# Performance work log

Hardware: AMD Instinct MI355X
Metric: run time of the kernel (lower is better)

## Reference

```python
import jax, jax.numpy as jnp
import numpy as np

H = 2048       # hidden_size
NH = 16        # num query heads
NKV = 4        # num key/value heads
HD = 128       # head_dim
EPS = 1e-6
ROPE_BASE = 10000.0


def rms_norm(x, w):
    xf = x.astype(jnp.float32)
    var = jnp.mean(xf * xf, axis=-1, keepdims=True)
    return (w * (xf * jax.lax.rsqrt(var + EPS)).astype(x.dtype))


def rope_cos_sin(seq_len, dtype):
    inv_freq = 1.0 / (ROPE_BASE ** (jnp.arange(0, HD, 2, dtype=jnp.float32) / HD))
    pos = jnp.arange(seq_len, dtype=jnp.float32)
    ang = pos[:, None] * inv_freq[None, :]            # [S, HD/2]
    emb = jnp.concatenate([ang, ang], axis=-1)        # [S, HD]
    return jnp.cos(emb).astype(dtype), jnp.sin(emb).astype(dtype)


def rotate_half(x):
    x1, x2 = jnp.split(x, 2, axis=-1)
    return jnp.concatenate([-x2, x1], axis=-1)


def setup_inputs() -> dict:
    key = jax.random.key(0)
    ks = jax.random.split(key, 8)
    B, S = 2, 2048
    hidden_states = jax.random.normal(ks[0], (B, S, H), dtype=jnp.float32)
    # additive causal mask [B,1,S,S]
    causal = jnp.where(jnp.tril(jnp.ones((S, S), dtype=bool)), 0.0, -1e9).astype(jnp.float32)
    attention_mask = jnp.broadcast_to(causal[None, None], (B, 1, S, S))
    sc = 1.0 / np.sqrt(H)
    Wq = jax.random.normal(ks[1], (NH * HD, H), dtype=jnp.float32) * sc
    Wk = jax.random.normal(ks[2], (NKV * HD, H), dtype=jnp.float32) * sc
    Wv = jax.random.normal(ks[3], (NKV * HD, H), dtype=jnp.float32) * sc
    Wo = jax.random.normal(ks[4], (H, NH * HD), dtype=jnp.float32) * sc
    q_norm_w = jnp.ones((HD,), dtype=jnp.float32)
    k_norm_w = jnp.ones((HD,), dtype=jnp.float32)
    return {"hidden_states": hidden_states, "attention_mask": attention_mask,
            "Wq": Wq, "Wk": Wk, "Wv": Wv, "Wo": Wo,
            "q_norm_w": q_norm_w, "k_norm_w": k_norm_w}


def reference(hidden_states, attention_mask, Wq, Wk, Wv, Wo, q_norm_w, k_norm_w):
    B, S, _ = hidden_states.shape
    # projections (nn.Linear: x @ W.T)
    q = (hidden_states @ Wq.T).reshape(B, S, NH, HD).transpose(0, 2, 1, 3)   # [B,NH,S,HD]
    k = (hidden_states @ Wk.T).reshape(B, S, NKV, HD).transpose(0, 2, 1, 3)  # [B,NKV,S,HD]
    v = (hidden_states @ Wv.T).reshape(B, S, NKV, HD).transpose(0, 2, 1, 3)
    # QK RMSNorm over head_dim
    q = rms_norm(q, q_norm_w)
    k = rms_norm(k, k_norm_w)
    # RoPE
    cos, sin = rope_cos_sin(S, q.dtype)        # [S,HD]
    q = q * cos + rotate_half(q) * sin
    k = k * cos + rotate_half(k) * sin
    # GQA: repeat kv heads
    n_rep = NH // NKV
    k = jnp.repeat(k, n_rep, axis=1)           # [B,NH,S,HD]
    v = jnp.repeat(v, n_rep, axis=1)
    # attention
    scores = jnp.einsum('bhqd,bhkd->bhqk', q, k) / np.sqrt(HD)
    scores = scores + attention_mask
    probs = jax.nn.softmax(scores, axis=-1)
    attn = jnp.einsum('bhqk,bhkd->bhqd', probs, v)
    attn = attn.transpose(0, 2, 1, 3).reshape(B, S, NH * HD)
    return attn @ Wo.T
```

## Files before the change

kernel.cpp:

```cpp
#include <hip/hip_runtime.h>
#include <math.h>

#define NH 16
#define NKV 4
#define HD 128
#define SEQ 2048
#define BATCH 2
#define EPSF 1e-6f
#define QKV 3072

typedef __attribute__((ext_vector_type(8))) short bf16x8;
typedef __attribute__((ext_vector_type(4))) short short4v;
typedef __attribute__((ext_vector_type(4))) float f32x4;

__device__ __forceinline__ short f2bf(float x) {
    unsigned u = __float_as_uint(x);
    u += 0x7fffu + ((u >> 16) & 1u);
    return (short)(u >> 16);
}
__device__ __forceinline__ float bf2f(short x) {
    return __uint_as_float((unsigned)(unsigned short)x << 16);
}

__device__ __forceinline__ void gll16(const short* g, short* l) {
    __builtin_amdgcn_global_load_lds(
        (const __attribute__((address_space(1))) unsigned*)g,
        (__attribute__((address_space(3))) unsigned*)l, 16, 0, 0);
}

__global__ __launch_bounds__(256)
void cast_all(const float* __restrict__ hs, const float* __restrict__ Wq,
              const float* __restrict__ Wk, const float* __restrict__ Wv,
              const float* __restrict__ Wo, short* __restrict__ hsb,
              short* __restrict__ wqkv, short* __restrict__ wob)
{
    const size_t MEG = 1024 * 1024;
    const int id = blockIdx.x;
    const float* s;
    short* d;
    size_t off;
    if (id < 8192)       { s = hs; d = hsb;            off = (size_t)id * 1024; }
    else if (id < 12288) { s = Wq; d = wqkv;           off = (size_t)(id - 8192) * 1024; }
    else if (id < 13312) { s = Wk; d = wqkv + 4 * MEG; off = (size_t)(id - 12288) * 1024; }
    else if (id < 14336) { s = Wv; d = wqkv + 5 * MEG; off = (size_t)(id - 13312) * 1024; }
    else                 { s = Wo; d = wob;            off = (size_t)(id - 14336) * 1024; }
    const size_t i = off + threadIdx.x * 4;
    float4 v = *(const float4*)(s + i);
    short4v o;
    o.x = f2bf(v.x); o.y = f2bf(v.y); o.z = f2bf(v.z); o.w = f2bf(v.w);
    *(short4v*)(d + i) = o;
}

template<bool OUT_BF16>
__global__ __launch_bounds__(256)
void gemm_nt_mfma(const short* __restrict__ A, const short* __restrict__ B,
                  void* __restrict__ Cv, int M, int N, int K)
{
    __shared__ short As[128 * 32];
    __shared__ short Bs[128 * 32];

    const int tid = threadIdx.x;
    const int w = tid >> 6, lane = tid & 63;
    const int quad = lane >> 4, ln = lane & 15;
    const int mw = (w >> 1) * 64, nw = (w & 1) * 64;
    const int m0 = blockIdx.y * 128, n0 = blockIdx.x * 128;

    const int srow = w * 16 + (lane >> 2);
    const int scol = (lane & 3) * 8;
    const short* Ag0 = A + (size_t)(m0 + srow) * K + scol;
    const short* Ag1 = Ag0 + (size_t)64 * K;
    const short* Bg0 = B + (size_t)(n0 + srow) * K + scol;
    const short* Bg1 = Bg0 + (size_t)64 * K;
    short* Al0 = &As[(w * 16) * 32];
    short* Al1 = &As[(w * 16 + 64) * 32];
    short* Bl0 = &Bs[(w * 16) * 32];
    short* Bl1 = &Bs[(w * 16 + 64) * 32];

    f32x4 acc[4][4];
    #pragma unroll
    for (int i = 0; i < 4; ++i)
        #pragma unroll
        for (int j = 0; j < 4; ++j)
            acc[i][j] = (f32x4){0.f, 0.f, 0.f, 0.f};

    for (int k0 = 0; k0 < K; k0 += 32) {
        __syncthreads();
        gll16(Ag0 + k0, Al0);
        gll16(Ag1 + k0, Al1);
        gll16(Bg0 + k0, Bl0);
        gll16(Bg1 + k0, Bl1);
        __syncthreads();

        bf16x8 af[4], bfr[4];
        #pragma unroll
        for (int i = 0; i < 4; ++i)
            af[i] = *(const bf16x8*)&As[(mw + i * 16 + ln) * 32 + quad * 8];
        #pragma unroll
        for (int j = 0; j < 4; ++j)
            bfr[j] = *(const bf16x8*)&Bs[(nw + j * 16 + ln) * 32 + quad * 8];
        #pragma unroll
        for (int i = 0; i < 4; ++i)
            #pragma unroll
            for (int j = 0; j < 4; ++j)
                acc[i][j] = __builtin_amdgcn_mfma_f32_16x16x32_bf16(
                    af[i], bfr[j], acc[i][j], 0, 0, 0);
    }

    #pragma unroll
    for (int i = 0; i < 4; ++i) {
        #pragma unroll
        for (int reg = 0; reg < 4; ++reg) {
            const int row = m0 + mw + i * 16 + quad * 4 + reg;
            const size_t base = (size_t)row * N + n0 + nw;
            #pragma unroll
            for (int j = 0; j < 4; ++j) {
                if (OUT_BF16)
                    ((short*)Cv)[base + j * 16 + ln] = f2bf(acc[i][j][reg]);
                else
                    ((float*)Cv)[base + j * 16 + ln] = acc[i][j][reg];
            }
        }
    }
}

__global__ __launch_bounds__(256)
void norm_rope_bf16(short* __restrict__ qkv, const float* __restrict__ qw,
                    const float* __restrict__ kw)
{
    const int wave = threadIdx.x >> 6;
    const int lane = threadIdx.x & 63;
    const long vec = (long)blockIdx.x * 4 + wave;
    const long NQ = (long)BATCH * SEQ * NH;

    short* base;
    const float* w;
    int s;
    if (vec < NQ) {
        const long token = vec / NH;
        const int h = (int)(vec % NH);
        s = (int)(token % SEQ);
        base = qkv + token * QKV + h * HD;
        w = qw;
    } else {
        const long t = vec - NQ;
        const long token = t / NKV;
        const int kvh = (int)(t % NKV);
        s = (int)(token % SEQ);
        base = qkv + token * QKV + 2048 + kvh * HD;
        w = kw;
    }

    float x0 = bf2f(base[lane]);
    float x1 = bf2f(base[lane + 64]);
    float ss = x0 * x0 + x1 * x1;
    #pragma unroll
    for (int off = 32; off; off >>= 1) ss += __shfl_xor(ss, off, 64);
    const float r = rsqrtf(ss * (1.0f / HD) + EPSF);
    x0 = x0 * r * w[lane];
    x1 = x1 * r * w[lane + 64];

    const float inv_freq = expf(-(float)lane * (logf(10000.0f) / 64.0f));
    const float ang = (float)s * inv_freq;
    const float c = cosf(ang);
    const float sn = sinf(ang);
    base[lane]      = f2bf(x0 * c - x1 * sn);
    base[lane + 64] = f2bf(x1 * c + x0 * sn);
}

__global__ __launch_bounds__(256)
void transpose_v(const short* __restrict__ qkv, short* __restrict__ vT)
{
    __shared__ short T[32][33];
    const int bx = blockIdx.x;
    const int st = bx & 63;
    const int dt = (bx >> 6) & 3;
    const int bk = bx >> 8;
    const int s0 = st * 32, d0 = dt * 32;
    const int tid = threadIdx.x;
    const long tok0 = (long)(bk >> 2) * SEQ + s0;
    const int kvh = bk & 3;

    const int rs = tid >> 3;
    const int rc = (tid & 7) * 4;
    short4v val = *(const short4v*)(qkv + (tok0 + rs) * QKV + 2560 + kvh * HD + d0 + rc);
    T[rc + 0][rs] = val.x; T[rc + 1][rs] = val.y;
    T[rc + 2][rs] = val.z; T[rc + 3][rs] = val.w;
    __syncthreads();

    const int wd = tid >> 3;
    const int wsc = (tid & 7) * 4;
    short4v ov;
    ov.x = T[wd][wsc + 0]; ov.y = T[wd][wsc + 1];
    ov.z = T[wd][wsc + 2]; ov.w = T[wd][wsc + 3];
    *(short4v*)(vT + ((size_t)bk * HD + d0 + wd) * SEQ + s0 + wsc) = ov;
}

__global__ __launch_bounds__(256)
void flash_attn_mfma(const short* __restrict__ qkv, const short* __restrict__ vT,
                     short* __restrict__ o)
{
    __shared__ short Ks[64][144];
    __shared__ short Vt[128][80];
    __shared__ short Ps[4][16][80];

    const int tid = threadIdx.x;
    const int w = tid >> 6;
    const int lane = tid & 63;
    const int quad = lane >> 4;
    const int ln = lane & 15;

    const int bx = blockIdx.x;
    const int pair = bx & 15;
    const int bh = bx >> 4;
    const int h = bh & 15;
    const int b = bh >> 4;
    const int kvh = h >> 2;
    const int qa = pair, qb = 31 - pair;
    const int rA = qa * 64 + w * 16;
    const int rB = qb * 64 + w * 16;

    const float SC = 0.08838834764831845f * 1.4426950408889634f;

    bf16x8 qfA[4], qfB[4];
    {
        const short* qra = qkv + (size_t)(b * SEQ + rA + ln) * QKV + h * HD;
        const short* qrb = qkv + (size_t)(b * SEQ + rB + ln) * QKV + h * HD;
        #pragma unroll
        for (int f = 0; f < 4; ++f) {
            qfA[f] = *(const bf16x8*)(qra + f * 32 + quad * 8);
            qfB[f] = *(const bf16x8*)(qrb + f * 32 + quad * 8);
        }
    }

    f32x4 OaA[8], OaB[8];
    #pragma unroll
    for (int dg = 0; dg < 8; ++dg) {
        OaA[dg] = (f32x4){0.f, 0.f, 0.f, 0.f};
        OaB[dg] = (f32x4){0.f, 0.f, 0.f, 0.f};
    }
    float mA = -1e30f, lA = 0.f, mB = -1e30f, lB = 0.f;

    const short* kbase = qkv + (size_t)(b * SEQ) * QKV + 2048 + kvh * HD;
    const short* vbase = vT + (size_t)(b * NKV + kvh) * HD * SEQ;

    auto process = [&](int k0, int rX, float& mX, float& lX,
                       const bf16x8* qf, f32x4* Oa) {
        if (k0 > rX + 15) return;
        f32x4 s[4];
        #pragma unroll
        for (int g = 0; g < 4; ++g) {
            f32x4 acc = (f32x4){0.f, 0.f, 0.f, 0.f};
            #pragma unroll
            for (int f = 0; f < 4; ++f) {
                bf16x8 kf = *(const bf16x8*)&Ks[g * 16 + ln][f * 32 + quad * 8];
                acc = __builtin_amdgcn_mfma_f32_16x16x32_bf16(kf, qf[f], acc, 0, 0, 0);
            }
            s[g] = acc;
        }
        if (k0 + 63 > rX) {
            const int qrow = rX + ln;
            #pragma unroll
            for (int g = 0; g < 4; ++g) {
                #pragma unroll
                for (int reg = 0; reg < 4; ++reg) {
                    const int key = k0 + g * 16 + quad * 4 + reg;
                    if (key > qrow) s[g][reg] = -1e30f;
                }
            }
        }
        float mt = s[0][0];
        #pragma unroll
        for (int g = 0; g < 4; ++g)
            #pragma unroll
            for (int reg = 0; reg < 4; ++reg)
                mt = fmaxf(mt, s[g][reg]);
        mt = fmaxf(mt, __shfl_xor(mt, 16, 64));
        mt = fmaxf(mt, __shfl_xor(mt, 32, 64));
        const float mnew = fmaxf(mX, mt);
        const float c1 = SC * mnew;
        const float alpha = exp2f(__builtin_fmaf(SC, mX, -c1));
        float ps = 0.f;
        #pragma unroll
        for (int g = 0; g < 4; ++g) {
            float p0 = exp2f(__builtin_fmaf(s[g][0], SC, -c1));
            float p1 = exp2f(__builtin_fmaf(s[g][1], SC, -c1));
            float p2 = exp2f(__builtin_fmaf(s[g][2], SC, -c1));
            float p3 = exp2f(__builtin_fmaf(s[g][3], SC, -c1));
            ps += (p0 + p1) + (p2 + p3);
            short4v pk;
            pk.x = f2bf(p0); pk.y = f2bf(p1); pk.z = f2bf(p2); pk.w = f2bf(p3);
            *(short4v*)&Ps[w][ln][g * 16 + quad * 4] = pk;
        }
        ps += __shfl_xor(ps, 16, 64);
        ps += __shfl_xor(ps, 32, 64);
        lX = lX * alpha + ps;
        mX = mnew;
        #pragma unroll
        for (int dg = 0; dg < 8; ++dg) {
            Oa[dg][0] *= alpha; Oa[dg][1] *= alpha;
            Oa[dg][2] *= alpha; Oa[dg][3] *= alpha;
        }
        __asm volatile("s_waitcnt lgkmcnt(0)" ::: "memory");
        bf16x8 pf0 = *(const bf16x8*)&Ps[w][ln][quad * 8];
        bf16x8 pf1 = *(const bf16x8*)&Ps[w][ln][32 + quad * 8];
        #pragma unroll
        for (int dg = 0; dg < 8; ++dg) {
            bf16x8 vf0 = *(const bf16x8*)&Vt[dg * 16 + ln][quad * 8];
            bf16x8 vf1 = *(const bf16x8*)&Vt[dg * 16 + ln][32 + quad * 8];
            Oa[dg] = __builtin_amdgcn_mfma_f32_16x16x32_bf16(vf0, pf0, Oa[dg], 0, 0, 0);
            Oa[dg] = __builtin_amdgcn_mfma_f32_16x16x32_bf16(vf1, pf1, Oa[dg], 0, 0, 0);
        }
    };

    for (int kt = 0; kt <= qb; ++kt) {
        const int k0 = kt * 64;
        __syncthreads();
        #pragma unroll
        for (int i = 0; i < 4; ++i) {
            const int e = tid + i * 256;
            const int key = e >> 4;
            const int dg = (e & 15) * 8;
            *(bf16x8*)&Ks[key][dg] =
                *(const bf16x8*)(kbase + (size_t)(k0 + key) * QKV + dg);
        }
        #pragma unroll
        for (int i = 0; i < 4; ++i) {
            const int e = tid + i * 256;
            const int d = e >> 3;
            const int kg = (e & 7) * 8;
            *(bf16x8*)&Vt[d][kg] =
                *(const bf16x8*)(vbase + (size_t)d * SEQ + k0 + kg);
        }
        __syncthreads();

        process(k0, rA, mA, lA, qfA, OaA);
        process(k0, rB, mB, lB, qfB, OaB);
    }

    {
        const float invA = 1.0f / lA;
        const float invB = 1.0f / lB;
        short* orA = o + ((size_t)(b * SEQ + rA + ln) * NH + h) * HD;
        short* orB = o + ((size_t)(b * SEQ + rB + ln) * NH + h) * HD;
        #pragma unroll
        for (int dg = 0; dg < 8; ++dg) {
            short4v oa, ob;
            oa.x = f2bf(OaA[dg][0] * invA); oa.y = f2bf(OaA[dg][1] * invA);
            oa.z = f2bf(OaA[dg][2] * invA); oa.w = f2bf(OaA[dg][3] * invA);
            ob.x = f2bf(OaB[dg][0] * invB); ob.y = f2bf(OaB[dg][1] * invB);
            ob.z = f2bf(OaB[dg][2] * invB); ob.w = f2bf(OaB[dg][3] * invB);
            *(short4v*)(orA + dg * 16 + quad * 4) = oa;
            *(short4v*)(orB + dg * 16 + quad * 4) = ob;
        }
    }
}

extern "C" void kernel_launch(void* const* d_in, const int* in_sizes, int n_in,
                              void* d_out, int out_size, void* d_ws, size_t ws_size,
                              hipStream_t stream)
{
    const float* hs = (const float*)d_in[0];
    const float* Wq = (const float*)d_in[2];
    const float* Wk = (const float*)d_in[3];
    const float* Wv = (const float*)d_in[4];
    const float* Wo = (const float*)d_in[5];
    const float* qw = (const float*)d_in[6];
    const float* kw = (const float*)d_in[7];
    float* out = (float*)d_out;

    const size_t MEG = 1024 * 1024;
    short* hsb  = (short*)d_ws;
    short* wqkv = hsb + 8 * MEG;
    short* wob  = wqkv + 6 * MEG;
    short* qkvb = wob + 4 * MEG;
    short* vT   = (short*)d_out;

    const int M = BATCH * SEQ;
    dim3 blk(256);

    cast_all<<<dim3(18432), blk, 0, stream>>>(hs, Wq, Wk, Wv, Wo, hsb, wqkv, wob);

    gemm_nt_mfma<true><<<dim3(QKV / 128, M / 128), blk, 0, stream>>>(
        hsb, wqkv, qkvb, M, QKV, 2048);

    norm_rope_bf16<<<dim3((BATCH * SEQ * (NH + NKV)) / 4), blk, 0, stream>>>(
        qkvb, qw, kw);

    transpose_v<<<dim3(2048), blk, 0, stream>>>(qkvb, vT);

    flash_attn_mfma<<<dim3(512), blk, 0, stream>>>(qkvb, vT, hsb);

    gemm_nt_mfma<false><<<dim3(2048 / 128, M / 128), blk, 0, stream>>>(
        hsb, wob, out, M, 2048, 2048);
}
```

Measured before the change: 366.7 us.

## Split attention query tiles across 8 waves and prefetch K/V into registers

The flash attention kernel now launches 512 threads per block. Each group of four waves owns one of the two paired query tiles, where before each wave processed both tiles in sequence. The K/V tile for the next iteration is loaded into registers while the current tile is computed, overlapping global memory latency with the MFMA work. BF16 packing now uses the HIP packed conversion intrinsic. The cost is a larger block with higher register pressure under launch_bounds(512,4), and the short-tile half of the block sits idle at barriers for the later iterations.

```diff
diff --git a/kernel.cpp b/kernel.cpp
--- a/kernel.cpp
+++ b/kernel.cpp
@@ -1,4 +1,5 @@
 #include <hip/hip_runtime.h>
+#include <hip/hip_bf16.h>
 #include <math.h>
 
 #define NH 16
@@ -20,6 +21,10 @@
 }
 __device__ __forceinline__ float bf2f(short x) {
     return __uint_as_float((unsigned)(unsigned short)x << 16);
+}
+__device__ __forceinline__ unsigned pkbf(float a, float b) {
+    __hip_bfloat162 h = __float22bfloat162_rn(float2{a, b});
+    unsigned r; __builtin_memcpy(&r, &h, 4); return r;
 }
 
 __device__ __forceinline__ void gll16(const short* g, short* l) {
@@ -195,19 +200,21 @@
     *(short4v*)(vT + ((size_t)bk * HD + d0 + wd) * SEQ + s0 + wsc) = ov;
 }
 
-__global__ __launch_bounds__(256)
+__global__ __launch_bounds__(512, 4)
 void flash_attn_mfma(const short* __restrict__ qkv, const short* __restrict__ vT,
                      short* __restrict__ o)
 {
     __shared__ short Ks[64][144];
     __shared__ short Vt[128][80];
-    __shared__ short Ps[4][16][80];
+    __shared__ short Ps[8][16][80];
 
     const int tid = threadIdx.x;
     const int w = tid >> 6;
     const int lane = tid & 63;
     const int quad = lane >> 4;
     const int ln = lane & 15;
+    const int side = w >> 2;
+    const int sw = w & 3;
 
     const int bx = blockIdx.x;
     const int pair = bx & 15;
@@ -216,141 +223,127 @@
     const int b = bh >> 4;
     const int kvh = h >> 2;
     const int qa = pair, qb = 31 - pair;
-    const int rA = qa * 64 + w * 16;
-    const int rB = qb * 64 + w * 16;
+    const int qX = side ? qb : qa;
+    const int rX = qX * 64 + sw * 16;
 
     const float SC = 0.08838834764831845f * 1.4426950408889634f;
 
-    bf16x8 qfA[4], qfB[4];
+    bf16x8 qf[4];
     {
-        const short* qra = qkv + (size_t)(b * SEQ + rA + ln) * QKV + h * HD;
-        const short* qrb = qkv + (size_t)(b * SEQ + rB + ln) * QKV + h * HD;
-        #pragma unroll
-        for (int f = 0; f < 4; ++f) {
-            qfA[f] = *(const bf16x8*)(qra + f * 32 + quad * 8);
-            qfB[f] = *(const bf16x8*)(qrb + f * 32 + quad * 8);
-        }
-    }
-
-    f32x4 OaA[8], OaB[8];
+        const short* qrow = qkv + (size_t)(b * SEQ + rX + ln) * QKV + h * HD;
+        #pragma unroll
+        for (int f = 0; f < 4; ++f)
+            qf[f] = *(const bf16x8*)(qrow + f * 32 + quad * 8);
+    }
+
+    f32x4 Oa[8];
     #pragma unroll
-    for (int dg = 0; dg < 8; ++dg) {
-        OaA[dg] = (f32x4){0.f, 0.f, 0.f, 0.f};
-        OaB[dg] = (f32x4){0.f, 0.f, 0.f, 0.f};
-    }
-    float mA = -1e30f, lA = 0.f, mB = -1e30f, lB = 0.f;
+    for (int dg = 0; dg < 8; ++dg) Oa[dg] = (f32x4){0.f, 0.f, 0.f, 0.f};
+    float mX = -1e30f, lX = 0.f;
 
     const short* kbase = qkv + (size_t)(b * SEQ) * QKV + 2048 + kvh * HD;
     const short* vbase = vT + (size_t)(b * NKV + kvh) * HD * SEQ;
 
-    auto process = [&](int k0, int rX, float& mX, float& lX,
-                       const bf16x8* qf, f32x4* Oa) {
-        if (k0 > rX + 15) return;
-        f32x4 s[4];
-        #pragma unroll
-        for (int g = 0; g < 4; ++g) {
-            f32x4 acc = (f32x4){0.f, 0.f, 0.f, 0.f};
-            #pragma unroll
-            for (int f = 0; f < 4; ++f) {
-                bf16x8 kf = *(const bf16x8*)&Ks[g * 16 + ln][f * 32 + quad * 8];
-                acc = __builtin_amdgcn_mfma_f32_16x16x32_bf16(kf, qf[f], acc, 0, 0, 0);
-            }
-            s[g] = acc;
-        }
-        if (k0 + 63 > rX) {
-            const int qrow = rX + ln;
-            #pragma unroll
-            for (int g = 0; g < 4; ++g) {
-                #pragma unroll
-                for (int reg = 0; reg < 4; ++reg) {
-                    const int key = k0 + g * 16 + quad * 4 + reg;
-                    if (key > qrow) s[g][reg] = -1e30f;
-                }
-            }
-        }
-        float mt = s[0][0];
-        #pragma unroll
-        for (int g = 0; g < 4; ++g)
-            #pragma unroll
-            for (int reg = 0; reg < 4; ++reg)
-                mt = fmaxf(mt, s[g][reg]);
-        mt = fmaxf(mt, __shfl_xor(mt, 16, 64));
-        mt = fmaxf(mt, __shfl_xor(mt, 32, 64));
-        const float mnew = fmaxf(mX, mt);
-        const float c1 = SC * mnew;
-        const float alpha = exp2f(__builtin_fmaf(SC, mX, -c1));
-        float ps = 0.f;
-        #pragma unroll
-        for (int g = 0; g < 4; ++g) {
-            float p0 = exp2f(__builtin_fmaf(s[g][0], SC, -c1));
-            float p1 = exp2f(__builtin_fmaf(s[g][1], SC, -c1));
-            float p2 = exp2f(__builtin_fmaf(s[g][2], SC, -c1));
-            float p3 = exp2f(__builtin_fmaf(s[g][3], SC, -c1));
-            ps += (p0 + p1) + (p2 + p3);
-            short4v pk;
-            pk.x = f2bf(p0); pk.y = f2bf(p1); pk.z = f2bf(p2); pk.w = f2bf(p3);
-            *(short4v*)&Ps[w][ln][g * 16 + quad * 4] = pk;
-        }
-        ps += __shfl_xor(ps, 16, 64);
-        ps += __shfl_xor(ps, 32, 64);
-        lX = lX * alpha + ps;
-        mX = mnew;
-        #pragma unroll
-        for (int dg = 0; dg < 8; ++dg) {
-            Oa[dg][0] *= alpha; Oa[dg][1] *= alpha;
-            Oa[dg][2] *= alpha; Oa[dg][3] *= alpha;
-        }
-        __asm volatile("s_waitcnt lgkmcnt(0)" ::: "memory");
-        bf16x8 pf0 = *(const bf16x8*)&Ps[w][ln][quad * 8];
-        bf16x8 pf1 = *(const bf16x8*)&Ps[w][ln][32 + quad * 8];
-        #pragma unroll
-        for (int dg = 0; dg < 8; ++dg) {
-            bf16x8 vf0 = *(const bf16x8*)&Vt[dg * 16 + ln][quad * 8];
-            bf16x8 vf1 = *(const bf16x8*)&Vt[dg * 16 + ln][32 + quad * 8];
-            Oa[dg] = __builtin_amdgcn_mfma_f32_16x16x32_bf16(vf0, pf0, Oa[dg], 0, 0, 0);
-            Oa[dg] = __builtin_amdgcn_mfma_f32_16x16x32_bf16(vf1, pf1, Oa[dg], 0, 0, 0);
+    bf16x8 kp[2], vp[2];
+    auto prefetch = [&](int k0) {
+        #pragma unroll
+        for (int i = 0; i < 2; ++i) {
+            const int e = tid + i * 512;
+            kp[i] = *(const bf16x8*)(kbase + (size_t)(k0 + (e >> 4)) * QKV + (e & 15) * 8);
+            vp[i] = *(const bf16x8*)(vbase + (size_t)(e >> 3) * SEQ + k0 + (e & 7) * 8);
         }
     };
+    prefetch(0);
 
     for (int kt = 0; kt <= qb; ++kt) {
         const int k0 = kt * 64;
         __syncthreads();
         #pragma unroll
-        for (int i = 0; i < 4; ++i) {
-            const int e = tid + i * 256;
-            const int key = e >> 4;
-            const int dg = (e & 15) * 8;
-            *(bf16x8*)&Ks[key][dg] =
-                *(const bf16x8*)(kbase + (size_t)(k0 + key) * QKV + dg);
-        }
-        #pragma unroll
-        for (int i = 0; i < 4; ++i) {
-            const int e = tid + i * 256;
-            const int d = e >> 3;
-            const int kg = (e & 7) * 8;
-            *(bf16x8*)&Vt[d][kg] =
-                *(const bf16x8*)(vbase + (size_t)d * SEQ + k0 + kg);
+        for (int i = 0; i < 2; ++i) {
+            const int e = tid + i * 512;
+            *(bf16x8*)&Ks[e >> 4][(e & 15) * 8] = kp[i];
+            *(bf16x8*)&Vt[e >> 3][(e & 7) * 8] = vp[i];
         }
         __syncthreads();
-
-        process(k0, rA, mA, lA, qfA, OaA);
-        process(k0, rB, mB, lB, qfB, OaB);
+        if (kt < qb) prefetch(k0 + 64);
+
+        if (kt <= qX) {
+            f32x4 s[4];
+            #pragma unroll
+            for (int g = 0; g < 4; ++g) {
+                f32x4 acc = (f32x4){0.f, 0.f, 0.f, 0.f};
+                #pragma unroll
+                for (int f = 0; f < 4; ++f) {
+                    bf16x8 kf = *(const bf16x8*)&Ks[g * 16 + ln][f * 32 + quad * 8];
+                    acc = __builtin_amdgcn_mfma_f32_16x16x32_bf16(kf, qf[f], acc, 0, 0, 0);
+                }
+                s[g] = acc;
+            }
+            if (kt == qX) {
+                const int qrow = rX + ln;
+                #pragma unroll
+                for (int g = 0; g < 4; ++g)
+                    #pragma unroll
+                    for (int reg = 0; reg < 4; ++reg) {
+                        const int key = k0 + g * 16 + quad * 4 + reg;
+                        if (key > qrow) s[g][reg] = -1e30f;
+                    }
+            }
+            float mt = s[0][0];
+            #pragma unroll
+            for (int g = 0; g < 4; ++g)
+                #pragma unroll
+                for (int reg = 0; reg < 4; ++reg)
+                    mt = fmaxf(mt, s[g][reg]);
+            mt = fmaxf(mt, __shfl_xor(mt, 16, 64));
+            mt = fmaxf(mt, __shfl_xor(mt, 32, 64));
+            const float mnew = fmaxf(mX, mt);
+            const float c1 = SC * mnew;
+            const float alpha = exp2f(__builtin_fmaf(SC, mX, -c1));
+            float ps = 0.f;
+            #pragma unroll
+            for (int g = 0; g < 4; ++g) {
+                float p0 = exp2f(__builtin_fmaf(s[g][0], SC, -c1));
+                float p1 = exp2f(__builtin_fmaf(s[g][1], SC, -c1));
+                float p2 = exp2f(__builtin_fmaf(s[g][2], SC, -c1));
+                float p3 = exp2f(__builtin_fmaf(s[g][3], SC, -c1));
+                ps += (p0 + p1) + (p2 + p3);
+                uint2 pk;
+                pk.x = pkbf(p0, p1);
+                pk.y = pkbf(p2, p3);
+                *(uint2*)&Ps[w][ln][g * 16 + quad * 4] = pk;
+            }
+            ps += __shfl_xor(ps, 16, 64);
+            ps += __shfl_xor(ps, 32, 64);
+            lX = lX * alpha + ps;
+            mX = mnew;
+            #pragma unroll
+            for (int dg = 0; dg < 8; ++dg) {
+                Oa[dg][0] *= alpha; Oa[dg][1] *= alpha;
+                Oa[dg][2] *= alpha; Oa[dg][3] *= alpha;
+            }
+            __asm volatile("s_waitcnt lgkmcnt(0)" ::: "memory");
+            bf16x8 pf0 = *(const bf16x8*)&Ps[w][ln][quad * 8];
+            bf16x8 pf1 = *(const bf16x8*)&Ps[w][ln][32 + quad * 8];
+            #pragma unroll
+            for (int dg = 0; dg < 8; ++dg) {
+                bf16x8 vf0 = *(const bf16x8*)&Vt[dg * 16 + ln][quad * 8];
+                bf16x8 vf1 = *(const bf16x8*)&Vt[dg * 16 + ln][32 + quad * 8];
+                Oa[dg] = __builtin_amdgcn_mfma_f32_16x16x32_bf16(vf0, pf0, Oa[dg], 0, 0, 0);
+                Oa[dg] = __builtin_amdgcn_mfma_f32_16x16x32_bf16(vf1, pf1, Oa[dg], 0, 0, 0);
+            }
+        }
     }
 
     {
-        const float invA = 1.0f / lA;
-        const float invB = 1.0f / lB;
-        short* orA = o + ((size_t)(b * SEQ + rA + ln) * NH + h) * HD;
-        short* orB = o + ((size_t)(b * SEQ + rB + ln) * NH + h) * HD;
+        const float inv = 1.0f / lX;
+        short* orow = o + ((size_t)(b * SEQ + rX + ln) * NH + h) * HD;
         #pragma unroll
         for (int dg = 0; dg < 8; ++dg) {
-            short4v oa, ob;
-            oa.x = f2bf(OaA[dg][0] * invA); oa.y = f2bf(OaA[dg][1] * invA);
-            oa.z = f2bf(OaA[dg][2] * invA); oa.w = f2bf(OaA[dg][3] * invA);
-            ob.x = f2bf(OaB[dg][0] * invB); ob.y = f2bf(OaB[dg][1] * invB);
-            ob.z = f2bf(OaB[dg][2] * invB); ob.w = f2bf(OaB[dg][3] * invB);
-            *(short4v*)(orA + dg * 16 + quad * 4) = oa;
-            *(short4v*)(orB + dg * 16 + quad * 4) = ob;
+            uint2 ov;
+            ov.x = pkbf(Oa[dg][0] * inv, Oa[dg][1] * inv);
+            ov.y = pkbf(Oa[dg][2] * inv, Oa[dg][3] * inv);
+            *(uint2*)(orow + dg * 16 + quad * 4) = ov;
         }
     }
 }
@@ -388,7 +381,7 @@
 
     transpose_v<<<dim3(2048), blk, 0, stream>>>(qkvb, vT);
 
-    flash_attn_mfma<<<dim3(512), blk, 0, stream>>>(qkvb, vT, hsb);
+    flash_attn_mfma<<<dim3(512), dim3(512), 0, stream>>>(qkvb, vT, hsb);
 
     gemm_nt_mfma<false><<<dim3(2048 / 128, M / 128), blk, 0, stream>>>(
         hsb, wob, out, M, 2048, 2048);
```

New measurement: 358.4 us. 1.02x faster.
